# Kernel tuning notes

Measured on AMD Instinct MI355X. Metric: run time of the kernel, lower is better.

## Reference

```python
import jax, jax.numpy as jnp
import numpy as np

N, E = 100000, 800000
IN, HID, H, C, L, OUT = 32, 128, 4, 32, 3, 5
NEG_SLOPE = 0.2
EPS = 1e-5


def setup_inputs() -> dict:
    key = jax.random.key(0)
    ks = jax.random.split(key, 20)
    s = 0.1
    inp = {
        "x": jax.random.normal(ks[0], (N, IN), jnp.float32),
        "edge_index": jax.random.randint(ks[1], (2, E), 0, N, jnp.int64),
        "edge_attr": jax.random.uniform(ks[2], (E, 1), jnp.float32),
        "Win": jax.random.normal(ks[3], (IN, HID), jnp.float32) * s,
        "b_in": jnp.zeros((HID,), jnp.float32),
        "Wg": jax.random.normal(ks[4], (L, HID, H * C), jnp.float32) * s,
        "bg": jnp.zeros((L, H * C), jnp.float32),
        "a_src": jax.random.normal(ks[5], (L, H, C), jnp.float32) * s,
        "a_dst": jax.random.normal(ks[6], (L, H, C), jnp.float32) * s,
        "We": jax.random.normal(ks[7], (L, 1, H * C), jnp.float32) * s,
        "a_edge": jax.random.normal(ks[8], (L, H, C), jnp.float32) * s,
        "ln_w": jnp.ones((L, HID), jnp.float32),
        "ln_b": jnp.zeros((L, HID), jnp.float32),
        "Wout": jax.random.normal(ks[9], (HID, OUT), jnp.float32) * s,
        "bout": jnp.zeros((OUT,), jnp.float32),
    }
    return inp


def _add_self_loops(src, dst, ea):
    # PyG fill_value='mean': self-loop attr = mean of incoming edge attrs per node
    ones = jnp.ones((src.shape[0],), ea.dtype)
    deg = jax.ops.segment_sum(ones, dst, N)
    loop_attr = jax.ops.segment_sum(ea, dst, N) / jnp.maximum(deg, 1.0)[:, None]
    idx = jnp.arange(N, dtype=src.dtype)
    return (jnp.concatenate([src, idx]), jnp.concatenate([dst, idx]),
            jnp.concatenate([ea, loop_attr], axis=0))


def _gat_conv(x, src, dst, ea, Wg, bg, a_s, a_d, We, a_e):
    xh = (x @ Wg).reshape(N, H, C)                    # [N,H,C]
    al_s = jnp.einsum('nhc,hc->nh', xh, a_s)          # [N,H]
    al_d = jnp.einsum('nhc,hc->nh', xh, a_d)
    ee = (ea @ We).reshape(-1, H, C)                  # [Et,H,C]
    al_e = jnp.einsum('ehc,hc->eh', ee, a_e)
    logits = jax.nn.leaky_relu(al_s[src] + al_d[dst] + al_e, NEG_SLOPE)
    m = jax.ops.segment_max(logits, dst, N)
    m = jnp.where(jnp.isfinite(m), m, 0.0)
    ex = jnp.exp(logits - m[dst])
    den = jax.ops.segment_sum(ex, dst, N)
    alpha = ex / (den[dst] + 1e-16)                   # segment softmax over dst
    out = jax.ops.segment_sum(alpha[:, :, None] * xh[src], dst, N)
    return out.reshape(N, H * C) + bg


def _graph_layernorm(h, w, b):
    # PyG LayerNorm(mode='graph'): normalize over all nodes and features
    h = h - jnp.mean(h)
    var = jnp.mean(h * h)
    return h / jnp.sqrt(var + EPS) * w + b


def reference(x, edge_index, edge_attr, Win, b_in, Wg, bg, a_src, a_dst, We,
              a_edge, ln_w, ln_b, Wout, bout):
    src, dst = edge_index[0], edge_index[1]
    src, dst, ea = _add_self_loops(src, dst, edge_attr)
    h = x @ Win + b_in
    for l in range(L):
        g = _gat_conv(h, src, dst, ea, Wg[l], bg[l], a_src[l], a_dst[l],
                      We[l], a_edge[l])
        g = _graph_layernorm(g, ln_w[l], ln_b[l])
        h = jax.nn.relu(g + h)
    return h @ Wout + bout
```

## Files before the change

### kernel.cpp

```cpp
#include <hip/hip_runtime.h>
#include <hip/hip_bf16.h>

#define NN 100000
#define EE 800000
#define HID 128
#define NH 4
#define CH 32
#define NL 3
#define NOUT 5
#define NEG_SLOPE 0.2f
#define LN_EPS 1e-5f
#define GCAP 96
#define NB_SCAN 98
#define HQ (HID / 2)
#define WB_LSZ 9216
#define NB_INIT 391

typedef unsigned int u32;
typedef __attribute__((ext_vector_type(8))) short bf16x8;
typedef __attribute__((ext_vector_type(4))) float f32x4;

static __device__ __forceinline__ float bflo(u32 r) { return __uint_as_float(r << 16); }
static __device__ __forceinline__ float bfhi(u32 r) { return __uint_as_float(r & 0xffff0000u); }
static __device__ __forceinline__ unsigned short f2bf(float x) {
    union U { __hip_bfloat16 b; unsigned short s; } u;
    u.b = __float2bfloat16(x);
    return u.s;
}
static __device__ __forceinline__ u32 pack2(float a, float b) {
    return (u32)f2bf(a) | ((u32)f2bf(b) << 16);
}
static __device__ __forceinline__ float lrelu(float x) {
    return x > 0.f ? x : NEG_SLOPE * x;
}

__global__ void prep_kernel(int* __restrict__ cnt, float* __restrict__ partials,
                            const float* __restrict__ We, const float* __restrict__ a_e,
                            float* __restrict__ wedot,
                            const float* __restrict__ Win, const float* __restrict__ b_in,
                            const float* __restrict__ Wg, float* __restrict__ wf,
                            const float* __restrict__ a_src, const float* __restrict__ a_dst,
                            u32* __restrict__ wb) {
    int b = blockIdx.x, t = threadIdx.x;
    if (b < NB_INIT) {
        int n = b * 256 + t;
        if (n < NN) cnt[n] = 1;
        if (n < 2048) partials[n] = 0.f;
        return;
    }
    if (b == NB_INIT) {
        if (t < NL * NH) {
            int l = t >> 2, hh = t & 3;
            float s = 0.f;
            #pragma unroll
            for (int c = 0; c < CH; c++)
                s += We[l * HID + hh * CH + c] * a_e[l * HID + hh * CH + c];
            wedot[t] = s;
        }
        return;
    }
    if (b < NB_INIT + 18) {
        int idx = (b - NB_INIT - 1) * 256 + t;
        if (idx >= 33 * HID) return;
        int r = idx >> 7, c = idx & 127;
        float acc = 0.f;
        for (int k = 0; k < HID; k++) {
            float a = (r < 32) ? Win[r * HID + k] : b_in[k];
            acc += a * Wg[(size_t)k * HID + c];
        }
        wf[r * HID + c] = acc;
        return;
    }
    {
        int idx = (b - NB_INIT - 18) * 256 + t;
        if (idx >= 2 * 2304) return;
        int l = idx / 2304;
        int rem = idx % 2304;
        int ks = rem / 576;
        int ct = (rem % 576) / 64;
        int lane = rem % 64;
        int q = lane >> 4, n = lane & 15;
        const float* W = Wg + (size_t)(l + 1) * HID * HID;
        float v[8];
        if (ct < 8) {
            #pragma unroll
            for (int j = 0; j < 8; j++) {
                int k = ks * 32 + q * 8 + j;
                v[j] = W[(size_t)k * HID + ct * 16 + n];
            }
        } else {
            #pragma unroll
            for (int j = 0; j < 8; j++) v[j] = 0.f;
            if (n < 8) {
                const float* a = (n < 4) ? (a_src + (l + 1) * HID + (n & 3) * CH)
                                         : (a_dst + (l + 1) * HID + (n & 3) * CH);
                #pragma unroll
                for (int j = 0; j < 8; j++) {
                    int k = ks * 32 + q * 8 + j;
                    const float* wrow = W + (size_t)k * HID + (n & 3) * CH;
                    float s = 0.f;
                    for (int c = 0; c < CH; c++) s += wrow[c] * a[c];
                    v[j] = s;
                }
            }
        }
        u32* dst = wb + (size_t)l * WB_LSZ + (size_t)((ks * 9 + ct) * 64 + lane) * 4;
        dst[0] = pack2(v[0], v[1]); dst[1] = pack2(v[2], v[3]);
        dst[2] = pack2(v[4], v[5]); dst[3] = pack2(v[6], v[7]);
    }
}

__global__ void hist_kernel(const int* __restrict__ ei, int* __restrict__ cnt,
                            int* __restrict__ slot) {
    int e = blockIdx.x * blockDim.x + threadIdx.x;
    if (e >= EE) return;
    int d = ei[EE + e];
    slot[e] = atomicAdd(&cnt[d], 1);
}

__global__ __launch_bounds__(1024) void scan1_kernel(const int* __restrict__ cnt,
                                                     int* __restrict__ rowptr,
                                                     int* __restrict__ bsum) {
    __shared__ int ws[16];
    int gid = blockIdx.x * 1024 + threadIdx.x;
    int v = (gid < NN) ? cnt[gid] : 0;
    int lane = threadIdx.x & 63, wid = threadIdx.x >> 6;
    int s = v;
    #pragma unroll
    for (int off = 1; off < 64; off <<= 1) {
        int t = __shfl_up(s, off, 64);
        if (lane >= off) s += t;
    }
    if (lane == 63) ws[wid] = s;
    __syncthreads();
    int add = 0;
    for (int w2 = 0; w2 < wid; w2++) add += ws[w2];
    int incl = s + add;
    if (gid <= NN) rowptr[gid] = incl - v;
    if (threadIdx.x == 1023) bsum[blockIdx.x] = incl;
}

__global__ void scan2_kernel(int* __restrict__ bsum) {
    __shared__ int w0tot;
    int tid = threadIdx.x;
    int v = (tid < NB_SCAN) ? bsum[tid] : 0;
    int lane = tid & 63, wid = tid >> 6;
    int s = v;
    #pragma unroll
    for (int off = 1; off < 64; off <<= 1) {
        int t = __shfl_up(s, off, 64);
        if (lane >= off) s += t;
    }
    if (wid == 0 && lane == 63) w0tot = s;
    __syncthreads();
    int incl = s + (wid ? w0tot : 0);
    if (tid < NB_SCAN) bsum[tid] = incl - v;
}

__global__ void scan3_kernel(int* __restrict__ rowptr, const int* __restrict__ bsum) {
    int gid = blockIdx.x * 1024 + threadIdx.x;
    if (gid <= NN) rowptr[gid] += bsum[blockIdx.x];
}

__global__ void scatter_kernel(const int* __restrict__ ei, const float* __restrict__ ea,
                               const int* __restrict__ rowptr, const int* __restrict__ slot,
                               uint2* __restrict__ edges) {
    int e = blockIdx.x * blockDim.x + threadIdx.x;
    if (e >= EE) return;
    int d = ei[EE + e];
    int pos = rowptr[d] + slot[e];
    edges[pos] = make_uint2((u32)ei[e], __float_as_uint(ea[e]));
}

__global__ void selfloop_kernel(const int* __restrict__ rowptr, uint2* __restrict__ edges) {
    int n = blockIdx.x * blockDim.x + threadIdx.x;
    if (n >= NN) return;
    int rs = rowptr[n], re = rowptr[n + 1];
    float s = 0.f;
    for (int i = rs + 1; i < re; i++) s += __uint_as_float(edges[i].y);
    float m = s / fmaxf((float)(re - rs - 1), 1.0f);
    edges[rs] = make_uint2((u32)n, __float_as_uint(m));
}

static __device__ __forceinline__ void store_xh_al(
        float acc[8][4], int n0, int r0, int c0, int cg,
        u32* __restrict__ xh, const float* __restrict__ asl, const float* __restrict__ adl,
        float* __restrict__ al_s, float* __restrict__ al_d) {
    float4 as4 = *(const float4*)&asl[c0];
    float4 ad4 = *(const float4*)&adl[c0];
    int hh = cg >> 3;
    #pragma unroll
    for (int i = 0; i < 8; i++) {
        int row = n0 + r0 + i;
        if (row < NN) {
            u32 lo = pack2(acc[i][0], acc[i][1]);
            u32 hi = pack2(acc[i][2], acc[i][3]);
            *(uint2*)&xh[(size_t)row * HQ + (c0 >> 1)] = make_uint2(lo, hi);
        }
        float ps = acc[i][0] * as4.x + acc[i][1] * as4.y + acc[i][2] * as4.z + acc[i][3] * as4.w;
        float pd = acc[i][0] * ad4.x + acc[i][1] * ad4.y + acc[i][2] * ad4.z + acc[i][3] * ad4.w;
        ps += __shfl_xor(ps, 1, 64); pd += __shfl_xor(pd, 1, 64);
        ps += __shfl_xor(ps, 2, 64); pd += __shfl_xor(pd, 2, 64);
        ps += __shfl_xor(ps, 4, 64); pd += __shfl_xor(pd, 4, 64);
        if ((cg & 7) == 0 && row < NN) {
            al_s[row * 4 + hh] = ps;
            al_d[row * 4 + hh] = pd;
        }
    }
}

__global__ __launch_bounds__(256) void in_gemm_kernel(
        const float* __restrict__ x, const float* __restrict__ Win,
        const float* __restrict__ b_in, const float* __restrict__ wf,
        u32* __restrict__ h, u32* __restrict__ xh,
        const float* __restrict__ a_src0, const float* __restrict__ a_dst0,
        float* __restrict__ al_s, float* __restrict__ al_d) {
    __shared__ float xs[64][36];
    __shared__ float ws[32][128];
    int n0 = blockIdx.x * 64;
    int t = threadIdx.x;
    int cg = t & 31, rg = t >> 5;
    int c0 = cg * 4, r0 = rg * 8;
    #pragma unroll
    for (int it = 0; it < 2; it++) {
        int idx = t + it * 256;
        int row = idx >> 3, kk = (idx & 7) * 4;
        float4 v = make_float4(0.f, 0.f, 0.f, 0.f);
        if (n0 + row < NN) v = *(const float4*)&x[(size_t)(n0 + row) * 32 + kk];
        *(float4*)&xs[row][kk] = v;
    }
    #pragma unroll
    for (int it = 0; it < 4; it++) {
        int idx = t + it * 256;
        int kr = idx >> 5, f4 = (idx & 31) * 4;
        *(float4*)&ws[kr][f4] = *(const float4*)&Win[kr * HID + f4];
    }
    __syncthreads();
    {
        float acc[8][4] = {};
        #pragma unroll 8
        for (int k = 0; k < 32; k++) {
            float4 b4 = *(const float4*)&ws[k][c0];
            #pragma unroll
            for (int i = 0; i < 8; i++) {
                float a = xs[r0 + i][k];
                acc[i][0] += a * b4.x; acc[i][1] += a * b4.y;
                acc[i][2] += a * b4.z; acc[i][3] += a * b4.w;
            }
        }
        float4 bi = *(const float4*)&b_in[c0];
        #pragma unroll
        for (int i = 0; i < 8; i++) {
            int row = n0 + r0 + i;
            if (row < NN) {
                u32 lo = pack2(acc[i][0] + bi.x, acc[i][1] + bi.y);
                u32 hi = pack2(acc[i][2] + bi.z, acc[i][3] + bi.w);
                *(uint2*)&h[(size_t)row * HQ + (c0 >> 1)] = make_uint2(lo, hi);
            }
        }
    }
    __syncthreads();
    #pragma unroll
    for (int it = 0; it < 4; it++) {
        int idx = t + it * 256;
        int kr = idx >> 5, f4 = (idx & 31) * 4;
        *(float4*)&ws[kr][f4] = *(const float4*)&wf[kr * HID + f4];
    }
    __syncthreads();
    float acc2[8][4] = {};
    #pragma unroll 8
    for (int k = 0; k < 32; k++) {
        float4 b4 = *(const float4*)&ws[k][c0];
        #pragma unroll
        for (int i = 0; i < 8; i++) {
            float a = xs[r0 + i][k];
            acc2[i][0] += a * b4.x; acc2[i][1] += a * b4.y;
            acc2[i][2] += a * b4.z; acc2[i][3] += a * b4.w;
        }
    }
    float4 bf4 = *(const float4*)&wf[32 * HID + c0];
    #pragma unroll
    for (int i = 0; i < 8; i++) {
        acc2[i][0] += bf4.x; acc2[i][1] += bf4.y; acc2[i][2] += bf4.z; acc2[i][3] += bf4.w;
    }
    store_xh_al(acc2, n0, r0, c0, cg, xh, a_src0, a_dst0, al_s, al_d);
}

__global__ __launch_bounds__(256) void gemm_mfma_kernel(const u32* __restrict__ h,
        const u32* __restrict__ wb, u32* __restrict__ xh, const u32* __restrict__ g,
        const float* __restrict__ lnw, const float* __restrict__ lnb,
        const float* __restrict__ stats, u32* __restrict__ hout,
        float* __restrict__ al_s, float* __restrict__ al_d) {
    __shared__ u32 hsu[4096];
    float mean = stats[0], rstd = stats[1];
    int n0 = blockIdx.x * 64;
    int t = threadIdx.x;
    int wv = t >> 6, lane = t & 63;
    int q = lane >> 4, n16 = lane & 15;

    bf16x8 bfrag[2][4];
    #pragma unroll
    for (int ks = 0; ks < 4; ks++) {
        #pragma unroll
        for (int cc = 0; cc < 2; cc++) {
            int ct = wv * 2 + cc;
            uint4 r = *(const uint4*)&wb[(size_t)((ks * 9 + ct) * 64 + lane) * 4];
            bfrag[cc][ks] = __builtin_bit_cast(bf16x8, r);
        }
    }
    bf16x8 bal[4];
    #pragma unroll
    for (int ks = 0; ks < 4; ks++) {
        uint4 r = *(const uint4*)&wb[(size_t)((ks * 9 + 8) * 64 + lane) * 4];
        bal[ks] = __builtin_bit_cast(bf16x8, r);
    }

    {
        int row = t >> 2;
        int qq = t & 3;
        int gr = n0 + row;
        int rt = row >> 4, m = row & 15;
        #pragma unroll
        for (int ks = 0; ks < 4; ks++) {
            int kk = ks * 32 + qq * 8;
            uint4 op = make_uint4(0u, 0u, 0u, 0u);
            if (gr < NN) {
                size_t base = (size_t)gr * HQ + (kk >> 1);
                uint4 gp = *(const uint4*)&g[base];
                uint4 hp = *(const uint4*)&h[base];
                float4 wA = *(const float4*)&lnw[kk];
                float4 wB = *(const float4*)&lnw[kk + 4];
                float4 bA = *(const float4*)&lnb[kk];
                float4 bB = *(const float4*)&lnb[kk + 4];
                float v0 = fmaxf((bflo(gp.x) - mean) * rstd * wA.x + bA.x + bflo(hp.x), 0.f);
                float v1 = fmaxf((bfhi(gp.x) - mean) * rstd * wA.y + bA.y + bfhi(hp.x), 0.f);
                float v2 = fmaxf((bflo(gp.y) - mean) * rstd * wA.z + bA.z + bflo(hp.y), 0.f);
                float v3 = fmaxf((bfhi(gp.y) - mean) * rstd * wA.w + bA.w + bfhi(hp.y), 0.f);
                float v4 = fmaxf((bflo(gp.z) - mean) * rstd * wB.x + bB.x + bflo(hp.z), 0.f);
                float v5 = fmaxf((bfhi(gp.z) - mean) * rstd * wB.y + bB.y + bfhi(hp.z), 0.f);
                float v6 = fmaxf((bflo(gp.w) - mean) * rstd * wB.z + bB.z + bflo(hp.w), 0.f);
                float v7 = fmaxf((bfhi(gp.w) - mean) * rstd * wB.w + bB.w + bfhi(hp.w), 0.f);
                op.x = pack2(v0, v1); op.y = pack2(v2, v3);
                op.z = pack2(v4, v5); op.w = pack2(v6, v7);
                *(uint4*)&hout[base] = op;
            }
            *(uint4*)&hsu[((rt * 4 + ks) * 64 + qq * 16 + m) * 4] = op;
        }
    }
    __syncthreads();

    f32x4 acc[4][2];
    f32x4 accal[4];
    #pragma unroll
    for (int rt = 0; rt < 4; rt++) {
        acc[rt][0] = (f32x4){0.f, 0.f, 0.f, 0.f};
        acc[rt][1] = (f32x4){0.f, 0.f, 0.f, 0.f};
        accal[rt]  = (f32x4){0.f, 0.f, 0.f, 0.f};
    }
    #pragma unroll
    for (int rt = 0; rt < 4; rt++) {
        #pragma unroll
        for (int ks = 0; ks < 4; ks++) {
            uint4 araw = *(const uint4*)&hsu[((rt * 4 + ks) * 64 + lane) * 4];
            bf16x8 af = __builtin_bit_cast(bf16x8, araw);
            acc[rt][0] = __builtin_amdgcn_mfma_f32_16x16x32_bf16(af, bfrag[0][ks], acc[rt][0], 0, 0, 0);
            acc[rt][1] = __builtin_amdgcn_mfma_f32_16x16x32_bf16(af, bfrag[1][ks], acc[rt][1], 0, 0, 0);
            if (wv == 3)
                accal[rt] = __builtin_amdgcn_mfma_f32_16x16x32_bf16(af, bal[ks], accal[rt], 0, 0, 0);
        }
    }

    #pragma unroll
    for (int rt = 0; rt < 4; rt++) {
        #pragma unroll
        for (int reg = 0; reg < 4; reg++) {
            int row = n0 + rt * 16 + q * 4 + reg;
            #pragma unroll
            for (int cc = 0; cc < 2; cc++) {
                float v = acc[rt][cc][reg];
                float vp = __shfl_xor(v, 1, 64);
                if (!(n16 & 1) && row < NN) {
                    int colp = (wv * 2 + cc) * 8 + (n16 >> 1);
                    xh[(size_t)row * HQ + colp] = pack2(v, vp);
                }
            }
            if (wv == 3 && row < NN && n16 < 8) {
                float v = accal[rt][reg];
                if (n16 < 4) al_s[row * 4 + n16] = v;
                else         al_d[row * 4 + (n16 - 4)] = v;
            }
        }
    }
}

__global__ __launch_bounds__(256) void gat_agg_kernel(const int* __restrict__ rowptr,
        const uint2* __restrict__ edges, const u32* __restrict__ xh,
        const float* __restrict__ al_s, const float* __restrict__ al_d,
        const float* __restrict__ wedot, const float* __restrict__ bg,
        u32* __restrict__ g, float* __restrict__ partials) {
    __shared__ float lds_ex[4][GCAP * 4];
    __shared__ int lds_src[4][GCAP];
    int wv = threadIdx.x >> 6, lane = threadIdx.x & 63;
    int base = (blockIdx.x * 4 + wv) * 4;
    if (base >= NN) return;
    float* ex_w = lds_ex[wv];
    int* src_w = lds_src[wv];
    int b1 = base + 1 < NN ? base + 1 : NN;
    int b2 = base + 2 < NN ? base + 2 : NN;
    int b3 = base + 3 < NN ? base + 3 : NN;
    int b4 = base + 4 < NN ? base + 4 : NN;
    int r0 = rowptr[base], r1 = rowptr[b1], r2 = rowptr[b2], r3 = rowptr[b3], r4 = rowptr[b4];
    int span = r4 - r0;
    int ncached = span < GCAP ? span : GCAP;
    float wd0 = wedot[0], wd1 = wedot[1], wd2 = wedot[2], wd3 = wedot[3];

    for (int i = lane; i < ncached; i += 64) {
        int gi = r0 + i;
        uint2 e = edges[gi];
        int s = (int)e.x;
        float eav = __uint_as_float(e.y);
        int d = (gi >= r1) + (gi >= r2) + (gi >= r3);
        float4 aldv = *(const float4*)&al_d[(base + d) * 4];
        float4 als = *(const float4*)&al_s[s * 4];
        float e0 = __expf(lrelu(als.x + aldv.x + eav * wd0));
        float e1 = __expf(lrelu(als.y + aldv.y + eav * wd1));
        float e2 = __expf(lrelu(als.z + aldv.z + eav * wd2));
        float e3 = __expf(lrelu(als.w + aldv.w + eav * wd3));
        src_w[i] = s;
        *(float4*)&ex_w[i * 4] = make_float4(e0, e1, e2, e3);
    }

    int nl = lane >> 4, cg = lane & 15;
    int n = base + nl;
    bool nvalid = n < NN;
    int ls = (nl == 0 ? r0 : nl == 1 ? r1 : nl == 2 ? r2 : r3) - r0;
    int le = (nl == 0 ? r1 : nl == 1 ? r2 : nl == 2 ? r3 : r4) - r0;
    int lec = le < ncached ? le : ncached;
    int head = cg >> 2;
    int c4 = cg * 4;
    float a0 = 0.f, a1 = 0.f, a2 = 0.f, a3 = 0.f;
    float a4 = 0.f, a5 = 0.f, a6 = 0.f, a7 = 0.f, den = 0.f;
    int j = ls;
    for (; j + 1 < lec; j += 2) {
        int s0 = src_w[j], s1 = src_w[j + 1];
        float e0 = ex_w[j * 4 + head], e1 = ex_w[(j + 1) * 4 + head];
        uint4 x0 = *(const uint4*)&xh[(size_t)s0 * HQ + c4];
        uint4 x1 = *(const uint4*)&xh[(size_t)s1 * HQ + c4];
        den += e0 + e1;
        a0 += e0 * bflo(x0.x); a1 += e0 * bfhi(x0.x);
        a2 += e0 * bflo(x0.y); a3 += e0 * bfhi(x0.y);
        a4 += e0 * bflo(x0.z); a5 += e0 * bfhi(x0.z);
        a6 += e0 * bflo(x0.w); a7 += e0 * bfhi(x0.w);
        a0 += e1 * bflo(x1.x); a1 += e1 * bfhi(x1.x);
        a2 += e1 * bflo(x1.y); a3 += e1 * bfhi(x1.y);
        a4 += e1 * bflo(x1.z); a5 += e1 * bfhi(x1.z);
        a6 += e1 * bflo(x1.w); a7 += e1 * bfhi(x1.w);
    }
    if (j < lec) {
        int s0 = src_w[j];
        float e0 = ex_w[j * 4 + head];
        uint4 x0 = *(const uint4*)&xh[(size_t)s0 * HQ + c4];
        den += e0;
        a0 += e0 * bflo(x0.x); a1 += e0 * bfhi(x0.x);
        a2 += e0 * bflo(x0.y); a3 += e0 * bfhi(x0.y);
        a4 += e0 * bflo(x0.z); a5 += e0 * bfhi(x0.z);
        a6 += e0 * bflo(x0.w); a7 += e0 * bfhi(x0.w);
        j++;
    }
    if (le > lec && nvalid) {
        float aldh = al_d[n * 4 + head];
        float wdh = wedot[head];
        for (int jt = (ls > lec ? ls : lec); jt < le; jt++) {
            uint2 e = edges[r0 + jt];
            int s = (int)e.x;
            float eav = __uint_as_float(e.y);
            float ex = __expf(lrelu(al_s[s * 4 + head] + aldh + eav * wdh));
            den += ex;
            uint4 x0 = *(const uint4*)&xh[(size_t)s * HQ + c4];
            a0 += ex * bflo(x0.x); a1 += ex * bfhi(x0.x);
            a2 += ex * bflo(x0.y); a3 += ex * bfhi(x0.y);
            a4 += ex * bflo(x0.z); a5 += ex * bfhi(x0.z);
            a6 += ex * bflo(x0.w); a7 += ex * bfhi(x0.w);
        }
    }

    float inv = 1.0f / (den + 1e-16f);
    int c0 = cg * 8;
    float4 bgA = *(const float4*)&bg[c0];
    float4 bgB = *(const float4*)&bg[c0 + 4];
    float o0 = a0 * inv + bgA.x, o1 = a1 * inv + bgA.y;
    float o2 = a2 * inv + bgA.z, o3 = a3 * inv + bgA.w;
    float o4 = a4 * inv + bgB.x, o5 = a5 * inv + bgB.y;
    float o6 = a6 * inv + bgB.z, o7 = a7 * inv + bgB.w;
    float ss = 0.f, sq = 0.f;
    if (nvalid) {
        uint4 op;
        op.x = pack2(o0, o1); op.y = pack2(o2, o3);
        op.z = pack2(o4, o5); op.w = pack2(o6, o7);
        *(uint4*)&g[(size_t)n * HQ + c4] = op;
        ss = o0 + o1 + o2 + o3 + o4 + o5 + o6 + o7;
        sq = o0 * o0 + o1 * o1 + o2 * o2 + o3 * o3
           + o4 * o4 + o5 * o5 + o6 * o6 + o7 * o7;
    }
    #pragma unroll
    for (int off = 1; off <= 32; off <<= 1) {
        ss += __shfl_xor(ss, off, 64);
        sq += __shfl_xor(sq, off, 64);
    }
    if (lane == 0) {
        int sl = ((blockIdx.x * 4 + wv) & 1023) * 2;
        atomicAdd(&partials[sl], ss);
        atomicAdd(&partials[sl + 1], sq);
    }
}

__global__ void stats_kernel(float* __restrict__ partials, float* __restrict__ stats) {
    __shared__ float ls[16], lq[16];
    int tid = threadIdx.x;
    float s = partials[tid * 2], q = partials[tid * 2 + 1];
    partials[tid * 2] = 0.f;
    partials[tid * 2 + 1] = 0.f;
    #pragma unroll
    for (int off = 32; off; off >>= 1) {
        s += __shfl_xor(s, off, 64);
        q += __shfl_xor(q, off, 64);
    }
    int lane = tid & 63, wid = tid >> 6;
    if (lane == 0) { ls[wid] = s; lq[wid] = q; }
    __syncthreads();
    if (tid == 0) {
        float S = 0.f, Q = 0.f;
        for (int w2 = 0; w2 < 16; w2++) { S += ls[w2]; Q += lq[w2]; }
        const float M = (float)NN * (float)HID;
        float mean = S / M;
        float var = Q / M - mean * mean;
        stats[0] = mean;
        stats[1] = rsqrtf(fmaxf(var, 0.f) + LN_EPS);
    }
}

__global__ __launch_bounds__(256) void ln_out_kernel(const u32* __restrict__ g,
        const u32* __restrict__ h, const float* __restrict__ lnw,
        const float* __restrict__ lnb, const float* __restrict__ stats,
        const float* __restrict__ Wout, const float* __restrict__ bout,
        float* __restrict__ out) {
    __shared__ float wsh[HID * NOUT];
    int t = threadIdx.x;
    for (int i = t; i < HID * NOUT; i += 256) wsh[i] = Wout[i];
    __syncthreads();
    int wv = t >> 6, lane = t & 63;
    int n = blockIdx.x * 4 + wv;
    if (n >= NN) return;
    float mean = stats[0], rstd = stats[1];
    int c0 = lane * 2;
    u32 gv = g[(size_t)n * HQ + lane];
    u32 hv = h[(size_t)n * HQ + lane];
    float o0 = fmaxf((bflo(gv) - mean) * rstd * lnw[c0]     + lnb[c0]     + bflo(hv), 0.f);
    float o1 = fmaxf((bfhi(gv) - mean) * rstd * lnw[c0 + 1] + lnb[c0 + 1] + bfhi(hv), 0.f);
    float p[NOUT];
    #pragma unroll
    for (int jj = 0; jj < NOUT; jj++)
        p[jj] = o0 * wsh[c0 * NOUT + jj] + o1 * wsh[(c0 + 1) * NOUT + jj];
    #pragma unroll
    for (int off = 32; off; off >>= 1) {
        #pragma unroll
        for (int jj = 0; jj < NOUT; jj++) p[jj] += __shfl_xor(p[jj], off, 64);
    }
    if (lane == 0) {
        #pragma unroll
        for (int jj = 0; jj < NOUT; jj++)
            out[(size_t)n * NOUT + jj] = p[jj] + bout[jj];
    }
}

extern "C" void kernel_launch(void* const* d_in, const int* in_sizes, int n_in,
                              void* d_out, int out_size, void* d_ws, size_t ws_size,
                              hipStream_t stream) {
    const float* x      = (const float*)d_in[0];
    const int*   ei     = (const int*)d_in[1];
    const float* ea     = (const float*)d_in[2];
    const float* Win    = (const float*)d_in[3];
    const float* b_in   = (const float*)d_in[4];
    const float* Wg     = (const float*)d_in[5];
    const float* bg     = (const float*)d_in[6];
    const float* a_src  = (const float*)d_in[7];
    const float* a_dst  = (const float*)d_in[8];
    const float* We     = (const float*)d_in[9];
    const float* a_edge = (const float*)d_in[10];
    const float* ln_w   = (const float*)d_in[11];
    const float* ln_b   = (const float*)d_in[12];
    const float* Wout   = (const float*)d_in[13];
    const float* bout   = (const float*)d_in[14];
    float* out = (float*)d_out;

    char* w = (char*)d_ws;
    size_t off = 0;
    auto alloc = [&](size_t bytes) -> void* {
        void* p = w + off;
        off = (off + bytes + 255) & ~(size_t)255;
        return p;
    };
    int*   slot    = (int*)alloc((size_t)EE * sizeof(int));
    int*   cnt     = (int*)alloc(NN * sizeof(int));
    int*   rowptr  = (int*)alloc((NN + 1) * sizeof(int));
    int*   bsum    = (int*)alloc(NB_SCAN * sizeof(int));
    uint2* edges   = (uint2*)alloc((size_t)(EE + NN) * sizeof(uint2));
    u32*   h       = (u32*)alloc((size_t)NN * HQ * sizeof(u32));
    u32*   g       = (u32*)alloc((size_t)NN * HQ * sizeof(u32));
    u32*   xh      = (u32*)alloc((size_t)NN * HQ * sizeof(u32));
    float* al_s    = (float*)alloc((size_t)NN * NH * sizeof(float));
    float* al_d    = (float*)alloc((size_t)NN * NH * sizeof(float));
    float* wedot   = (float*)alloc(16 * sizeof(float));
    float* wf      = (float*)alloc(33 * HID * sizeof(float));
    u32*   wb      = (u32*)alloc((size_t)2 * WB_LSZ * sizeof(u32));
    float* partials = (float*)alloc(2048 * sizeof(float));
    float* stats   = (float*)alloc(16 * sizeof(float));
    (void)ws_size; (void)n_in; (void)in_sizes; (void)out_size;

    prep_kernel<<<NB_INIT + 18 + 18, 256, 0, stream>>>(cnt, partials, We, a_edge, wedot,
                                                       Win, b_in, Wg, wf, a_src, a_dst, wb);
    hist_kernel<<<(EE + 255) / 256, 256, 0, stream>>>(ei, cnt, slot);
    scan1_kernel<<<NB_SCAN, 1024, 0, stream>>>(cnt, rowptr, bsum);
    scan2_kernel<<<1, 128, 0, stream>>>(bsum);
    scan3_kernel<<<NB_SCAN, 1024, 0, stream>>>(rowptr, bsum);
    scatter_kernel<<<(EE + 255) / 256, 256, 0, stream>>>(ei, ea, rowptr, slot, edges);
    selfloop_kernel<<<(NN + 255) / 256, 256, 0, stream>>>(rowptr, edges);

    const int ngrid = (NN + 63) / 64;
    in_gemm_kernel<<<ngrid, 256, 0, stream>>>(x, Win, b_in, wf, h, xh,
                                              a_src, a_dst, al_s, al_d);
    for (int l = 0; l < NL; l++) {
        if (l > 0) {
            gemm_mfma_kernel<<<ngrid, 256, 0, stream>>>(
                h, wb + (size_t)(l - 1) * WB_LSZ, xh, g,
                ln_w + (size_t)(l - 1) * HID, ln_b + (size_t)(l - 1) * HID, stats, h,
                al_s, al_d);
        }
        gat_agg_kernel<<<(NN + 15) / 16, 256, 0, stream>>>(
            rowptr, edges, xh, al_s, al_d, wedot + l * 4,
            bg + (size_t)l * HID, g, partials);
        stats_kernel<<<1, 1024, 0, stream>>>(partials, stats);
    }

    ln_out_kernel<<<(NN + 3) / 4, 256, 0, stream>>>(g, h, ln_w + (size_t)2 * HID,
                                                    ln_b + (size_t)2 * HID,
                                                    stats, Wout, bout, out);
}
```

Measured before the change: 417.2 us.

## Fold LN stats into gemm, pack slot with dst, unroll aggregation, vectorize output

Per-layer stats kernels are removed. Each gemm_mfma block now reduces the previous layer's partial sums itself, and separate partial buffers per layer remove the need to zero them between launches. hist now packs the destination id with the slot, so scatter no longer rereads edge_index. The GAT gather loop is unrolled by 4 to keep more loads in flight, and ln_out processes 4 nodes per wave with vector loads. The slot packing assumes in-degree below 256 and node ids below 2^24. Each gemm block also redoes the 2048-element reduction.

```diff
diff --git a/kernel.cpp b/kernel.cpp
--- a/kernel.cpp
+++ b/kernel.cpp
@@ -45,7 +45,7 @@
     if (b < NB_INIT) {
         int n = b * 256 + t;
         if (n < NN) cnt[n] = 1;
-        if (n < 2048) partials[n] = 0.f;
+        if (n < 3 * 2048) partials[n] = 0.f;
         return;
     }
     if (b == NB_INIT) {
@@ -111,11 +111,12 @@
 }
 
 __global__ void hist_kernel(const int* __restrict__ ei, int* __restrict__ cnt,
-                            int* __restrict__ slot) {
+                            u32* __restrict__ slot) {
     int e = blockIdx.x * blockDim.x + threadIdx.x;
     if (e >= EE) return;
     int d = ei[EE + e];
-    slot[e] = atomicAdd(&cnt[d], 1);
+    int s = atomicAdd(&cnt[d], 1);
+    slot[e] = ((u32)d << 8) | (u32)s;
 }
 
 __global__ __launch_bounds__(1024) void scan1_kernel(const int* __restrict__ cnt,
@@ -163,12 +164,13 @@
 }
 
 __global__ void scatter_kernel(const int* __restrict__ ei, const float* __restrict__ ea,
-                               const int* __restrict__ rowptr, const int* __restrict__ slot,
+                               const int* __restrict__ rowptr, const u32* __restrict__ slot,
                                uint2* __restrict__ edges) {
     int e = blockIdx.x * blockDim.x + threadIdx.x;
     if (e >= EE) return;
-    int d = ei[EE + e];
-    int pos = rowptr[d] + slot[e];
+    u32 p = slot[e];
+    int d = (int)(p >> 8);
+    int pos = rowptr[d] + (int)(p & 255u);
     edges[pos] = make_uint2((u32)ei[e], __float_as_uint(ea[e]));
 }
 
@@ -289,14 +291,33 @@
 __global__ __launch_bounds__(256) void gemm_mfma_kernel(const u32* __restrict__ h,
         const u32* __restrict__ wb, u32* __restrict__ xh, const u32* __restrict__ g,
         const float* __restrict__ lnw, const float* __restrict__ lnb,
-        const float* __restrict__ stats, u32* __restrict__ hout,
+        const float* __restrict__ partials, u32* __restrict__ hout,
         float* __restrict__ al_s, float* __restrict__ al_d) {
     __shared__ u32 hsu[4096];
-    float mean = stats[0], rstd = stats[1];
+    __shared__ float sred[8];
     int n0 = blockIdx.x * 64;
     int t = threadIdx.x;
     int wv = t >> 6, lane = t & 63;
     int q = lane >> 4, n16 = lane & 15;
+
+    {
+        const float4* pp = (const float4*)partials;
+        float4 v0 = pp[t * 2], v1 = pp[t * 2 + 1];
+        float s = v0.x + v0.z + v1.x + v1.z;
+        float qq = v0.y + v0.w + v1.y + v1.w;
+        #pragma unroll
+        for (int off = 1; off <= 32; off <<= 1) {
+            s += __shfl_xor(s, off, 64);
+            qq += __shfl_xor(qq, off, 64);
+        }
+        if (lane == 0) { sred[wv * 2] = s; sred[wv * 2 + 1] = qq; }
+    }
+    __syncthreads();
+    float S = sred[0] + sred[2] + sred[4] + sred[6];
+    float Q = sred[1] + sred[3] + sred[5] + sred[7];
+    const float M = (float)NN * (float)HID;
+    float mean = S / M;
+    float rstd = rsqrtf(fmaxf(Q / M - mean * mean, 0.f) + LN_EPS);
 
     bf16x8 bfrag[2][4];
     #pragma unroll
@@ -441,12 +462,15 @@
     float a0 = 0.f, a1 = 0.f, a2 = 0.f, a3 = 0.f;
     float a4 = 0.f, a5 = 0.f, a6 = 0.f, a7 = 0.f, den = 0.f;
     int j = ls;
-    for (; j + 1 < lec; j += 2) {
-        int s0 = src_w[j], s1 = src_w[j + 1];
-        float e0 = ex_w[j * 4 + head], e1 = ex_w[(j + 1) * 4 + head];
+    for (; j + 3 < lec; j += 4) {
+        int s0 = src_w[j], s1 = src_w[j + 1], s2 = src_w[j + 2], s3 = src_w[j + 3];
+        float e0 = ex_w[j * 4 + head],       e1 = ex_w[(j + 1) * 4 + head];
+        float e2 = ex_w[(j + 2) * 4 + head], e3 = ex_w[(j + 3) * 4 + head];
         uint4 x0 = *(const uint4*)&xh[(size_t)s0 * HQ + c4];
         uint4 x1 = *(const uint4*)&xh[(size_t)s1 * HQ + c4];
-        den += e0 + e1;
+        uint4 x2 = *(const uint4*)&xh[(size_t)s2 * HQ + c4];
+        uint4 x3 = *(const uint4*)&xh[(size_t)s3 * HQ + c4];
+        den += e0 + e1 + e2 + e3;
         a0 += e0 * bflo(x0.x); a1 += e0 * bfhi(x0.x);
         a2 += e0 * bflo(x0.y); a3 += e0 * bfhi(x0.y);
         a4 += e0 * bflo(x0.z); a5 += e0 * bfhi(x0.z);
@@ -455,8 +479,16 @@
         a2 += e1 * bflo(x1.y); a3 += e1 * bfhi(x1.y);
         a4 += e1 * bflo(x1.z); a5 += e1 * bfhi(x1.z);
         a6 += e1 * bflo(x1.w); a7 += e1 * bfhi(x1.w);
-    }
-    if (j < lec) {
+        a0 += e2 * bflo(x2.x); a1 += e2 * bfhi(x2.x);
+        a2 += e2 * bflo(x2.y); a3 += e2 * bfhi(x2.y);
+        a4 += e2 * bflo(x2.z); a5 += e2 * bfhi(x2.z);
+        a6 += e2 * bflo(x2.w); a7 += e2 * bfhi(x2.w);
+        a0 += e3 * bflo(x3.x); a1 += e3 * bfhi(x3.x);
+        a2 += e3 * bflo(x3.y); a3 += e3 * bfhi(x3.y);
+        a4 += e3 * bflo(x3.z); a5 += e3 * bfhi(x3.z);
+        a6 += e3 * bflo(x3.w); a7 += e3 * bfhi(x3.w);
+    }
+    for (; j < lec; j++) {
         int s0 = src_w[j];
         float e0 = ex_w[j * 4 + head];
         uint4 x0 = *(const uint4*)&xh[(size_t)s0 * HQ + c4];
@@ -465,7 +497,6 @@
         a2 += e0 * bflo(x0.y); a3 += e0 * bfhi(x0.y);
         a4 += e0 * bflo(x0.z); a5 += e0 * bfhi(x0.z);
         a6 += e0 * bflo(x0.w); a7 += e0 * bfhi(x0.w);
-        j++;
     }
     if (le > lec && nvalid) {
         float aldh = al_d[n * 4 + head];
@@ -514,12 +545,10 @@
     }
 }
 
-__global__ void stats_kernel(float* __restrict__ partials, float* __restrict__ stats) {
+__global__ void stats_kernel(const float* __restrict__ partials, float* __restrict__ stats) {
     __shared__ float ls[16], lq[16];
     int tid = threadIdx.x;
     float s = partials[tid * 2], q = partials[tid * 2 + 1];
-    partials[tid * 2] = 0.f;
-    partials[tid * 2 + 1] = 0.f;
     #pragma unroll
     for (int off = 32; off; off >>= 1) {
         s += __shfl_xor(s, off, 64);
@@ -549,24 +578,40 @@
     for (int i = t; i < HID * NOUT; i += 256) wsh[i] = Wout[i];
     __syncthreads();
     int wv = t >> 6, lane = t & 63;
-    int n = blockIdx.x * 4 + wv;
-    if (n >= NN) return;
+    int nl = lane >> 4, cg = lane & 15;
+    int n = (blockIdx.x * 4 + wv) * 4 + nl;
+    bool nvalid = n < NN;
     float mean = stats[0], rstd = stats[1];
-    int c0 = lane * 2;
-    u32 gv = g[(size_t)n * HQ + lane];
-    u32 hv = h[(size_t)n * HQ + lane];
-    float o0 = fmaxf((bflo(gv) - mean) * rstd * lnw[c0]     + lnb[c0]     + bflo(hv), 0.f);
-    float o1 = fmaxf((bfhi(gv) - mean) * rstd * lnw[c0 + 1] + lnb[c0 + 1] + bfhi(hv), 0.f);
-    float p[NOUT];
-    #pragma unroll
-    for (int jj = 0; jj < NOUT; jj++)
-        p[jj] = o0 * wsh[c0 * NOUT + jj] + o1 * wsh[(c0 + 1) * NOUT + jj];
-    #pragma unroll
-    for (int off = 32; off; off >>= 1) {
+    float p[NOUT] = {};
+    if (nvalid) {
+        int c0 = cg * 8;
+        uint4 gv = *(const uint4*)&g[(size_t)n * HQ + cg * 4];
+        uint4 hv = *(const uint4*)&h[(size_t)n * HQ + cg * 4];
+        float4 wA = *(const float4*)&lnw[c0], wB = *(const float4*)&lnw[c0 + 4];
+        float4 bA = *(const float4*)&lnb[c0], bB = *(const float4*)&lnb[c0 + 4];
+        float o[8];
+        o[0] = fmaxf((bflo(gv.x) - mean) * rstd * wA.x + bA.x + bflo(hv.x), 0.f);
+        o[1] = fmaxf((bfhi(gv.x) - mean) * rstd * wA.y + bA.y + bfhi(hv.x), 0.f);
+        o[2] = fmaxf((bflo(gv.y) - mean) * rstd * wA.z + bA.z + bflo(hv.y), 0.f);
+        o[3] = fmaxf((bfhi(gv.y) - mean) * rstd * wA.w + bA.w + bfhi(hv.y), 0.f);
+        o[4] = fmaxf((bflo(gv.z) - mean) * rstd * wB.x + bB.x + bflo(hv.z), 0.f);
+        o[5] = fmaxf((bfhi(gv.z) - mean) * rstd * wB.y + bB.y + bfhi(hv.z), 0.f);
+        o[6] = fmaxf((bflo(gv.w) - mean) * rstd * wB.z + bB.z + bflo(hv.w), 0.f);
+        o[7] = fmaxf((bfhi(gv.w) - mean) * rstd * wB.w + bB.w + bfhi(hv.w), 0.f);
+        #pragma unroll
+        for (int jj = 0; jj < NOUT; jj++) {
+            float acc = 0.f;
+            #pragma unroll
+            for (int k = 0; k < 8; k++) acc += o[k] * wsh[(c0 + k) * NOUT + jj];
+            p[jj] = acc;
+        }
+    }
+    #pragma unroll
+    for (int off = 1; off <= 8; off <<= 1) {
         #pragma unroll
         for (int jj = 0; jj < NOUT; jj++) p[jj] += __shfl_xor(p[jj], off, 64);
     }
-    if (lane == 0) {
+    if (cg == 0 && nvalid) {
         #pragma unroll
         for (int jj = 0; jj < NOUT; jj++)
             out[(size_t)n * NOUT + jj] = p[jj] + bout[jj];
@@ -600,7 +645,7 @@
         off = (off + bytes + 255) & ~(size_t)255;
         return p;
     };
-    int*   slot    = (int*)alloc((size_t)EE * sizeof(int));
+    u32*   slot    = (u32*)alloc((size_t)EE * sizeof(u32));
     int*   cnt     = (int*)alloc(NN * sizeof(int));
     int*   rowptr  = (int*)alloc((NN + 1) * sizeof(int));
     int*   bsum    = (int*)alloc(NB_SCAN * sizeof(int));
@@ -613,7 +658,7 @@
     float* wedot   = (float*)alloc(16 * sizeof(float));
     float* wf      = (float*)alloc(33 * HID * sizeof(float));
     u32*   wb      = (u32*)alloc((size_t)2 * WB_LSZ * sizeof(u32));
-    float* partials = (float*)alloc(2048 * sizeof(float));
+    float* partials = (float*)alloc(3 * 2048 * sizeof(float));
     float* stats   = (float*)alloc(16 * sizeof(float));
     (void)ws_size; (void)n_in; (void)in_sizes; (void)out_size;
 
@@ -633,16 +678,16 @@
         if (l > 0) {
             gemm_mfma_kernel<<<ngrid, 256, 0, stream>>>(
                 h, wb + (size_t)(l - 1) * WB_LSZ, xh, g,
-                ln_w + (size_t)(l - 1) * HID, ln_b + (size_t)(l - 1) * HID, stats, h,
-                al_s, al_d);
+                ln_w + (size_t)(l - 1) * HID, ln_b + (size_t)(l - 1) * HID,
+                partials + (size_t)(l - 1) * 2048, h, al_s, al_d);
         }
         gat_agg_kernel<<<(NN + 15) / 16, 256, 0, stream>>>(
             rowptr, edges, xh, al_s, al_d, wedot + l * 4,
-            bg + (size_t)l * HID, g, partials);
-        stats_kernel<<<1, 1024, 0, stream>>>(partials, stats);
-    }
-
-    ln_out_kernel<<<(NN + 3) / 4, 256, 0, stream>>>(g, h, ln_w + (size_t)2 * HID,
-                                                    ln_b + (size_t)2 * HID,
-                                                    stats, Wout, bout, out);
-}
+            bg + (size_t)l * HID, g, partials + (size_t)l * 2048);
+    }
+    stats_kernel<<<1, 1024, 0, stream>>>(partials + 2 * 2048, stats);
+
+    ln_out_kernel<<<(NN + 15) / 16, 256, 0, stream>>>(g, h, ln_w + (size_t)2 * HID,
+                                                      ln_b + (size_t)2 * HID,
+                                                      stats, Wout, bout, out);
+}
```

Result: faster. 402.6 us (-3.5%).
